# Optimization experiments

Measured on AMD Instinct MI355X. Metric: run time of the kernel, lower is better.

The kernel has to match this reference:

```python
import jax, jax.numpy as jnp
import numpy as np

B, L, H, F = 8, 1024, 512, 4

def setup_inputs() -> dict:
    key = jax.random.key(0)
    ks = jax.random.split(key, 5)
    x = jax.random.normal(ks[0], (B, L, H), dtype=jnp.float32)
    x_mask = jax.random.randint(ks[1], (B, L), 0, 2).astype(jnp.int32)
    W_proj = jax.random.normal(ks[2], (H, H * F), dtype=jnp.float32) * (1.0 / np.sqrt(H))
    b_proj = jnp.zeros((H * F,), dtype=jnp.float32)
    W_gate = jax.random.normal(ks[3], (2 * H, 2 * H), dtype=jnp.float32) * (1.0 / np.sqrt(2 * H))
    b_gate = jnp.zeros((2 * H,), dtype=jnp.float32)
    return {"x": x, "x_mask": x_mask, "W_proj": W_proj, "b_proj": b_proj,
            "W_gate": W_gate, "b_gate": b_gate}

def masked_softmax(logits, mask, eps=1e-13):
    # allennlp-style masked softmax used throughout sgnlp:
    # softmax(logits * mask) * mask, renormalized.
    m = mask.astype(logits.dtype)
    p = jax.nn.softmax(logits * m, axis=-1) * m
    return p / (p.sum(axis=-1, keepdims=True) + eps)

def reference(x, x_mask, W_proj, b_proj, W_gate, b_gate):
    b, l, h = x.shape
    # multi-factor projection: (B,L,H) -> (B,L,H,F) with relu (Linear activation='relu', dropout=0)
    y = jax.nn.relu(jnp.einsum('blh,hk->blk', x, W_proj) + b_proj)
    y = y.reshape(b, l, h, F)
    # per-factor self-attn scores stacked on last axis: (B,L,L,F)
    scores = jnp.einsum('blhf,bmhf->blmf', y, y)
    self_attn = scores.max(axis=-1)  # attn_pooling == 'max'
    # pairwise mask, zero diagonal
    mask = x_mask[:, :, None] * x_mask[:, None, :]
    mask = mask * (1 - jnp.eye(l, dtype=mask.dtype))
    alpha = masked_softmax(self_attn, mask)
    multi_attn_enc = jnp.einsum('blm,bmh->blh', alpha, x)
    joint = jnp.concatenate([x, multi_attn_enc], axis=-1)  # (B,L,2H)
    gate = jax.nn.sigmoid(jnp.einsum('blk,kj->blj', joint, W_gate) + b_gate)
    return gate * joint
```

## Files before the change

kernel.cpp:

```cpp
#include <hip/hip_runtime.h>


typedef _Float16 half8 __attribute__((ext_vector_type(8)));
typedef float floatx4 __attribute__((ext_vector_type(4)));

typedef const __attribute__((address_space(1))) void* gas_ptr;
typedef __attribute__((address_space(3))) void* las_ptr;

#define WAITV(n) asm volatile("s_waitcnt vmcnt(" #n ") lgkmcnt(0)" ::: "memory")


template<int NCH, int NT>
__device__ __forceinline__ void init_ptrs(const _Float16* src, int row0, int ld,
                                          const _Float16* gp[NCH]) {
  int t = threadIdx.x;
#pragma unroll
  for (int p = 0; p < NCH; ++p) {
    int c = p * NT + t;
    int row = c >> 3;
    int kg = c & 7;
    int gk = (kg ^ (row & 7)) << 3;
    gp[p] = src + (size_t)(row0 + row) * ld + gk;
  }
}


template<int NCH, int NT>
__device__ __forceinline__ void init_ptrs32(const _Float16* src, int row0, int ld,
                                            const _Float16* gp[NCH]) {
  int t = threadIdx.x;
#pragma unroll
  for (int p = 0; p < NCH; ++p) {
    int c = p * NT + t;
    int pair = c >> 3, s = c & 7;
    int q = s ^ (pair & 7);
    int row = row0 + pair * 2 + (q >> 2);
    int gk = (q & 3) << 3;
    gp[p] = src + (size_t)row * ld + gk;
  }
}

template<int NCH, int NT>
__device__ __forceinline__ void stage(const _Float16* const gp[NCH], _Float16* ldsbuf) {
  int t = threadIdx.x;
#pragma unroll
  for (int p = 0; p < NCH; ++p)
    __builtin_amdgcn_global_load_lds((gas_ptr)gp[p],
                                     (las_ptr)(ldsbuf + t * 8 + p * NT * 8), 16, 0, 0);
}

template<int NCH>
__device__ __forceinline__ void bump(const _Float16* gp[NCH], int d) {
#pragma unroll
  for (int p = 0; p < NCH; ++p) gp[p] += d;
}

__device__ __forceinline__ half8 frag_ld(const _Float16* lds, int row, int g) {
  return *(const half8*)(lds + row * 64 + ((g ^ (row & 7)) << 3));
}

__device__ __forceinline__ half8 frag_ld32(const _Float16* lds, int row, int kg) {
  int pair = row >> 1;
  int slot = (kg | ((row & 1) << 2)) ^ (pair & 7);
  return *(const half8*)(lds + pair * 64 + slot * 8);
}

__device__ __forceinline__ void kstep44(const _Float16* la, const _Float16* lb,
                                        floatx4 (&acc)[4][4], int ra, int rb, int quad) {
  half8 af[4], bf[4];
#pragma unroll
  for (int mi = 0; mi < 4; ++mi) af[mi] = frag_ld32(la, ra + mi * 16, quad);
#pragma unroll
  for (int ni = 0; ni < 4; ++ni) bf[ni] = frag_ld32(lb, rb + ni * 16, quad);
  __builtin_amdgcn_s_setprio(1);
#pragma unroll
  for (int mi = 0; mi < 4; ++mi)
#pragma unroll
    for (int ni = 0; ni < 4; ++ni)
      acc[mi][ni] = __builtin_amdgcn_mfma_f32_16x16x32_f16(af[mi], bf[ni], acc[mi][ni], 0, 0, 0);
  __builtin_amdgcn_s_setprio(0);
}

__device__ __forceinline__ void mfma_tile42(const _Float16* la, const _Float16* lb,
                                            floatx4 acc[4][2], int wm, int wn,
                                            int l16, int quad) {
#pragma unroll
  for (int kf = 0; kf < 2; ++kf) {
    half8 af[4], bf[2];
#pragma unroll
    for (int i = 0; i < 4; ++i) af[i] = frag_ld(la, wm * 64 + i * 16 + l16, kf * 4 + quad);
#pragma unroll
    for (int i = 0; i < 2; ++i) bf[i] = frag_ld(lb, wn * 32 + i * 16 + l16, kf * 4 + quad);
#pragma unroll
    for (int mi = 0; mi < 4; ++mi)
#pragma unroll
      for (int ni = 0; ni < 2; ++ni)
        acc[mi][ni] = __builtin_amdgcn_mfma_f32_16x16x32_f16(af[mi], bf[ni], acc[mi][ni], 0, 0, 0);
  }
}

#define ZERO_ACC44(acc)                                 \
  _Pragma("unroll") for (int mi = 0; mi < 4; ++mi)      \
  _Pragma("unroll") for (int ni = 0; ni < 4; ++ni)      \
  _Pragma("unroll") for (int r = 0; r < 4; ++r) acc[mi][ni][r] = 0.0f;

#define ZERO_ACC42(acc)                                 \
  _Pragma("unroll") for (int mi = 0; mi < 4; ++mi)      \
  _Pragma("unroll") for (int ni = 0; ni < 2; ++ni)      \
  _Pragma("unroll") for (int r = 0; r < 4; ++r) acc[mi][ni][r] = 0.0f;


__global__ __launch_bounds__(256) void prep_kernel(const float* __restrict__ xin,
                                                   _Float16* __restrict__ x16,
                                                   _Float16* __restrict__ xT,
                                                   const float* __restrict__ Wp,
                                                   _Float16* __restrict__ WpT,
                                                   const float* __restrict__ Wg,
                                                   _Float16* __restrict__ WgT) {
  __shared__ float tile[32][33];
  int id = blockIdx.x;
  int tx = threadIdx.x & 31, ty = threadIdx.x >> 5;
  if (id < 4096) {
    const int R = 1024, C = 512;
    int b = id & 7, rest = id >> 3;
    int c0 = (rest & 15) * 32, r0 = (rest >> 4) * 32;
    size_t boff = (size_t)b * R * C;
    const float* in = xin + boff;
    _Float16* o16 = x16 + boff;
    _Float16* oT = xT + boff;
#pragma unroll
    for (int i = 0; i < 32; i += 8) {
      float v = in[(size_t)(r0 + ty + i) * C + c0 + tx];
      tile[ty + i][tx] = v;
      o16[(size_t)(r0 + ty + i) * C + c0 + tx] = (_Float16)v;
    }
    __syncthreads();
#pragma unroll
    for (int i = 0; i < 32; i += 8)
      oT[(size_t)(c0 + ty + i) * R + r0 + tx] = (_Float16)tile[tx][ty + i];
  } else {
    int w = id - 4096;
    int bx = w & 63, by = (w >> 6) & 15, bz = w >> 10;
    const float* in; _Float16* out; int R, C, c0, r0;
    if (bz == 0) {
      in = Wp; out = WpT; R = 512; C = 2048;
      c0 = bx * 32; r0 = by * 32;
    } else {
      in = Wg; out = WgT; R = 1024; C = 1024;
      c0 = (bx & 31) * 32; r0 = (by * 2 + (bx >> 5)) * 32;
    }
#pragma unroll
    for (int i = 0; i < 32; i += 8)
      tile[ty + i][tx] = in[(size_t)(r0 + ty + i) * C + c0 + tx];
    __syncthreads();
#pragma unroll
    for (int i = 0; i < 32; i += 8) {
      int rr = c0 + ty + i;
      int prow = (bz == 0) ? ((rr & 3) * 512 + (rr >> 2)) : rr;
      out[(size_t)prow * R + r0 + tx] = (_Float16)tile[tx][ty + i];
    }
  }
}


__global__ __launch_bounds__(256, 2) void proj_kernel(const _Float16* __restrict__ x16,
                                                      const _Float16* __restrict__ WpT,
                                                      const float* __restrict__ bp,
                                                      _Float16* __restrict__ y_t) {
  __shared__ __align__(16) _Float16 ldsA[4][128 * 32];
  __shared__ __align__(16) _Float16 ldsB[4][128 * 32];
  int id = blockIdx.x;
  int xcd = id & 7, r = id >> 3;
  int i0 = (xcd * 8 + (r & 7)) * 128;
  int n0 = (r >> 3) * 128;
  int t = threadIdx.x, lane = t & 63, w = t >> 6;
  int wm = w >> 1, wn = w & 1, quad = lane >> 4, l16 = lane & 15;
  int ra = wm * 64 + l16, rb = wn * 64 + l16;
  const _Float16* gpA[2]; const _Float16* gpB[2];
  init_ptrs32<2, 256>(x16, i0, 512, gpA);
  init_ptrs32<2, 256>(WpT, n0, 512, gpB);
  floatx4 acc[4][4];
  ZERO_ACC44(acc);
  stage<2, 256>(gpA, ldsA[0]); bump<2>(gpA, 32);
  stage<2, 256>(gpB, ldsB[0]); bump<2>(gpB, 32);
  stage<2, 256>(gpA, ldsA[1]); bump<2>(gpA, 32);
  stage<2, 256>(gpB, ldsB[1]); bump<2>(gpB, 32);
  stage<2, 256>(gpA, ldsA[2]); bump<2>(gpA, 32);
  stage<2, 256>(gpB, ldsB[2]); bump<2>(gpB, 32);
#pragma unroll 1
  for (int u = 0; u < 13; ++u) {
    WAITV(8);
    __builtin_amdgcn_s_barrier();
    stage<2, 256>(gpA, ldsA[(u + 3) & 3]); bump<2>(gpA, 32);
    stage<2, 256>(gpB, ldsB[(u + 3) & 3]); bump<2>(gpB, 32);
    kstep44(ldsA[u & 3], ldsB[u & 3], acc, ra, rb, quad);
  }
  WAITV(8); __builtin_amdgcn_s_barrier(); kstep44(ldsA[1], ldsB[1], acc, ra, rb, quad);
  WAITV(4); __builtin_amdgcn_s_barrier(); kstep44(ldsA[2], ldsB[2], acc, ra, rb, quad);
  WAITV(0); __builtin_amdgcn_s_barrier(); kstep44(ldsA[3], ldsB[3], acc, ra, rb, quad);
#pragma unroll
  for (int mi = 0; mi < 4; ++mi)
#pragma unroll
    for (int ni = 0; ni < 4; ++ni)
#pragma unroll
      for (int r2 = 0; r2 < 4; ++r2) {
        int gr = i0 + wm * 64 + mi * 16 + quad * 4 + r2;
        int gc = n0 + wn * 64 + ni * 16 + l16;
        int f = gc >> 9, h = gc & 511;
        float c = fmaxf(acc[mi][ni][r2] + bp[h * 4 + f], 0.0f);
        int b = gr >> 10, l = gr & 1023;
        y_t[(((size_t)(b * 4 + f)) * 1024 + l) * 512 + h] = (_Float16)c;
      }
}


__global__ __launch_bounds__(256, 3) void score_kernel(const _Float16* __restrict__ y_t,
                                                       float* __restrict__ S) {
  __shared__ __align__(16) char smem[49152];
  _Float16* LA0 = (_Float16*)smem;
  _Float16* LA1 = (_Float16*)(smem + 16384);
  _Float16* LB0 = (_Float16*)(smem + 32768);
  _Float16* LB1 = (_Float16*)(smem + 40960);
  int id = blockIdx.x;
  int b = id & 7;
  int tt = id >> 3;
  int ti = 0;
  while (tt >= 16 - 2 * ti) { tt -= 16 - 2 * ti; ++ti; }
  int jh = 2 * ti + tt;
  int i0 = ti * 128, j0 = jh * 64;
  int t = threadIdx.x, lane = t & 63, w = t >> 6;
  int wm = w >> 1, wn = w & 1, quad = lane >> 4, l16 = lane & 15;
  const int PLANE = 1024 * 512;
  const _Float16* base = y_t + (size_t)b * 4 * PLANE;
  const _Float16* gpA[4]; const _Float16* gpB[2];
  init_ptrs<4, 256>(base, i0, 512, gpA);
  init_ptrs<2, 256>(base, j0, 512, gpB);
  floatx4 acc[4][2], smax[4][2];
  ZERO_ACC42(acc);
  stage<4, 256>(gpA, LA0); bump<4>(gpA, 64);
  stage<2, 256>(gpB, LB0); bump<2>(gpB, 64);
#pragma unroll 1
  for (int f = 0; f < 4; ++f) {
#pragma unroll 1
    for (int kt = 0; kt < 8; ++kt) {
      __syncthreads();
      if (f * 8 + kt < 31) {
        if (kt == 7) { bump<4>(gpA, PLANE - 512); bump<2>(gpB, PLANE - 512); }
        stage<4, 256>(gpA, ((kt + 1) & 1) ? LA1 : LA0); bump<4>(gpA, 64);
        stage<2, 256>(gpB, ((kt + 1) & 1) ? LB1 : LB0); bump<2>(gpB, 64);
      }
      mfma_tile42((kt & 1) ? LA1 : LA0, (kt & 1) ? LB1 : LB0, acc, wm, wn, l16, quad);
    }
    if (f == 0) {
#pragma unroll
      for (int mi = 0; mi < 4; ++mi)
#pragma unroll
        for (int ni = 0; ni < 2; ++ni) smax[mi][ni] = acc[mi][ni];
    } else {
#pragma unroll
      for (int mi = 0; mi < 4; ++mi)
#pragma unroll
        for (int ni = 0; ni < 2; ++ni)
#pragma unroll
          for (int r = 0; r < 4; ++r)
            smax[mi][ni][r] = fmaxf(smax[mi][ni][r], acc[mi][ni][r]);
    }
    ZERO_ACC42(acc);
  }
  float* Sb = S + (size_t)b * 1024 * 1024;
#pragma unroll
  for (int mi = 0; mi < 4; ++mi)
#pragma unroll
    for (int ni = 0; ni < 2; ++ni)
#pragma unroll
      for (int r = 0; r < 4; ++r) {
        int gi = i0 + wm * 64 + mi * 16 + quad * 4 + r;
        int gj = j0 + wn * 32 + ni * 16 + l16;
        Sb[(size_t)gi * 1024 + gj] = smax[mi][ni][r];
      }
  if (jh >= 2 * ti + 2) {
    __syncthreads();
    float* tl = (float*)smem;
#pragma unroll
    for (int mi = 0; mi < 4; ++mi)
#pragma unroll
      for (int ni = 0; ni < 2; ++ni)
#pragma unroll
        for (int r = 0; r < 4; ++r)
          tl[(wm * 64 + mi * 16 + quad * 4 + r) * 65 + (wn * 32 + ni * 16 + l16)] =
              smax[mi][ni][r];
    __syncthreads();
#pragma unroll 1
    for (int k = 0; k < 32; ++k) {
      int flat = k * 256 + t;
      int rm = flat >> 7, cm = flat & 127;
      Sb[(size_t)(j0 + rm) * 1024 + (i0 + cm)] = tl[cm * 65 + rm];
    }
  }
}


__global__ __launch_bounds__(256) void softmax_kernel(const float* __restrict__ S,
                                                      const int* __restrict__ xmask,
                                                      _Float16* __restrict__ alpha) {
  __shared__ float red[16];
  int id = blockIdx.x;
  int b = id & 7, l = id >> 3;
  int row = b * 1024 + l;
  const float* sr = S + (size_t)row * 1024;
  const int* mr = xmask + b * 1024;
  int t = threadIdx.x, lane = t & 63, wid = t >> 6;
  int rm = mr[l];
  float v[4], mm[4];
  float vmax = 0.0f;
#pragma unroll
  for (int q = 0; q < 4; ++q) {
    int i = t + q * 256;
    int m = (rm && mr[i] && (i != l)) ? 1 : 0;
    mm[q] = (float)m;
    v[q] = m ? sr[i] : 0.0f;
    vmax = fmaxf(vmax, v[q]);
  }
  for (int off = 32; off; off >>= 1) vmax = fmaxf(vmax, __shfl_down(vmax, off));
  if (lane == 0) red[wid] = vmax;
  __syncthreads();
  if (t == 0) red[8] = fmaxf(fmaxf(red[0], red[1]), fmaxf(red[2], red[3]));
  __syncthreads();
  vmax = red[8];
  float e[4], E = 0.0f, E2 = 0.0f;
#pragma unroll
  for (int q = 0; q < 4; ++q) {
    e[q] = expf(v[q] - vmax);
    E += e[q];
    E2 += e[q] * mm[q];
  }
  for (int off = 32; off; off >>= 1) {
    E += __shfl_down(E, off);
    E2 += __shfl_down(E2, off);
  }
  if (lane == 0) { red[wid] = E; red[4 + wid] = E2; }
  __syncthreads();
  if (t == 0) {
    red[9] = red[0] + red[1] + red[2] + red[3];
    red[10] = red[4] + red[5] + red[6] + red[7];
  }
  __syncthreads();
  E = red[9]; E2 = red[10];
  float inv = 1.0f / (E2 + 1e-13f * E);
  _Float16* ar = alpha + (size_t)row * 1024;
#pragma unroll
  for (int q = 0; q < 4; ++q) {
    int i = t + q * 256;
    ar[i] = (_Float16)(e[q] * mm[q] * inv);
  }
}


__global__ __launch_bounds__(256) void attn_kernel(const _Float16* __restrict__ alpha,
                                                   const _Float16* __restrict__ xT,
                                                   _Float16* __restrict__ enc) {
  __shared__ __align__(16) _Float16 ldsA[2][64 * 64];
  __shared__ __align__(16) _Float16 ldsB[2][128 * 64];
  int id = blockIdx.x;
  int b = id & 7;
  int r2 = id >> 3;
  int i0 = (r2 >> 2) * 64;
  int n0 = (r2 & 3) * 128;
  const _Float16* A = alpha + (size_t)b * 1024 * 1024;
  const _Float16* Bm = xT + (size_t)b * 512 * 1024;
  int t = threadIdx.x, lane = t & 63, wn = t >> 6;
  int quad = lane >> 4, l16 = lane & 15;
  const _Float16* gpA[2]; const _Float16* gpB[4];
  init_ptrs<2, 256>(A, i0, 1024, gpA);
  init_ptrs<4, 256>(Bm, n0, 1024, gpB);
  floatx4 acc[4][2];
  ZERO_ACC42(acc);
  stage<2, 256>(gpA, ldsA[0]); bump<2>(gpA, 64);
  stage<4, 256>(gpB, ldsB[0]); bump<4>(gpB, 64);
#pragma unroll 1
  for (int kt = 0; kt < 16; ++kt) {
    __syncthreads();
    if (kt < 15) {
      stage<2, 256>(gpA, ldsA[(kt + 1) & 1]); bump<2>(gpA, 64);
      stage<4, 256>(gpB, ldsB[(kt + 1) & 1]); bump<4>(gpB, 64);
    }
    const _Float16* la = ldsA[kt & 1];
    const _Float16* lb = ldsB[kt & 1];
#pragma unroll
    for (int kf = 0; kf < 2; ++kf) {
      half8 af[4], bf[2];
#pragma unroll
      for (int i = 0; i < 4; ++i) af[i] = frag_ld(la, i * 16 + l16, kf * 4 + quad);
#pragma unroll
      for (int i = 0; i < 2; ++i) bf[i] = frag_ld(lb, wn * 32 + i * 16 + l16, kf * 4 + quad);
#pragma unroll
      for (int mi = 0; mi < 4; ++mi)
#pragma unroll
        for (int ni = 0; ni < 2; ++ni)
          acc[mi][ni] = __builtin_amdgcn_mfma_f32_16x16x32_f16(af[mi], bf[ni], acc[mi][ni], 0, 0, 0);
    }
  }
  _Float16* eb = enc + (size_t)b * 1024 * 512;
#pragma unroll
  for (int mi = 0; mi < 4; ++mi)
#pragma unroll
    for (int ni = 0; ni < 2; ++ni)
#pragma unroll
      for (int r = 0; r < 4; ++r) {
        int gr = i0 + mi * 16 + quad * 4 + r;
        int gc = n0 + wn * 32 + ni * 16 + l16;
        eb[(size_t)gr * 512 + gc] = (_Float16)acc[mi][ni][r];
      }
}


__global__ __launch_bounds__(256, 2) void gate_kernel(const _Float16* __restrict__ x16,
                                                      const _Float16* __restrict__ enc,
                                                      const _Float16* __restrict__ WgT,
                                                      const float* __restrict__ bg,
                                                      float* __restrict__ out) {
  __shared__ __align__(16) _Float16 ldsA[4][128 * 32];
  __shared__ __align__(16) _Float16 ldsB[4][128 * 32];
  int id = blockIdx.x;
  int xcd = id & 7, r = id >> 3;
  int i0 = (xcd * 8 + (r & 7)) * 128;
  int n0 = (r >> 3) * 128;
  int t = threadIdx.x, lane = t & 63, w = t >> 6;
  int wm = w >> 1, wn = w & 1, quad = lane >> 4, l16 = lane & 15;
  int ra = wm * 64 + l16, rb = wn * 64 + l16;
  const _Float16* gpA[2]; const _Float16* gpA2[2]; const _Float16* gpB[2];
  init_ptrs32<2, 256>(x16, i0, 512, gpA);
  init_ptrs32<2, 256>(enc, i0, 512, gpA2);
  init_ptrs32<2, 256>(WgT, n0, 1024, gpB);
  floatx4 acc[4][4];
  ZERO_ACC44(acc);
  stage<2, 256>(gpA, ldsA[0]); bump<2>(gpA, 32);
  stage<2, 256>(gpB, ldsB[0]); bump<2>(gpB, 32);
  stage<2, 256>(gpA, ldsA[1]); bump<2>(gpA, 32);
  stage<2, 256>(gpB, ldsB[1]); bump<2>(gpB, 32);
  stage<2, 256>(gpA, ldsA[2]); bump<2>(gpA, 32);
  stage<2, 256>(gpB, ldsB[2]); bump<2>(gpB, 32);
#pragma unroll 1
  for (int u = 0; u < 29; ++u) {
    WAITV(8);
    __builtin_amdgcn_s_barrier();
    int v = u + 3;
    if (v < 16) { stage<2, 256>(gpA,  ldsA[v & 3]); bump<2>(gpA, 32); }
    else        { stage<2, 256>(gpA2, ldsA[v & 3]); bump<2>(gpA2, 32); }
    stage<2, 256>(gpB, ldsB[v & 3]); bump<2>(gpB, 32);
    kstep44(ldsA[u & 3], ldsB[u & 3], acc, ra, rb, quad);
  }
  WAITV(8); __builtin_amdgcn_s_barrier(); kstep44(ldsA[1], ldsB[1], acc, ra, rb, quad);
  WAITV(4); __builtin_amdgcn_s_barrier(); kstep44(ldsA[2], ldsB[2], acc, ra, rb, quad);
  WAITV(0); __builtin_amdgcn_s_barrier(); kstep44(ldsA[3], ldsB[3], acc, ra, rb, quad);
#pragma unroll
  for (int mi = 0; mi < 4; ++mi)
#pragma unroll
    for (int ni = 0; ni < 4; ++ni)
#pragma unroll
      for (int r2 = 0; r2 < 4; ++r2) {
        int gr = i0 + wm * 64 + mi * 16 + quad * 4 + r2;
        int gc = n0 + wn * 64 + ni * 16 + l16;
        float c = acc[mi][ni][r2] + bg[gc];
        float g = 1.0f / (1.0f + expf(-c));
        float jv = (gc < 512) ? (float)x16[(size_t)gr * 512 + gc]
                              : (float)enc[(size_t)gr * 512 + (gc - 512)];
        out[(size_t)gr * 1024 + gc] = g * jv;
      }
}


extern "C" void kernel_launch(void* const* d_in, const int* in_sizes, int n_in,
                              void* d_out, int out_size, void* d_ws, size_t ws_size,
                              hipStream_t stream) {
  const float* x  = (const float*)d_in[0];
  const int* xm   = (const int*)d_in[1];
  const float* Wp = (const float*)d_in[2];
  const float* bp = (const float*)d_in[3];
  const float* Wg = (const float*)d_in[4];
  const float* bg = (const float*)d_in[5];
  float* out = (float*)d_out;

  char* ws = (char*)d_ws;
  const size_t MB = 1024 * 1024;
  _Float16* x16 = (_Float16*)(ws);
  _Float16* xT  = (_Float16*)(ws + 8 * MB);
  _Float16* WpT = (_Float16*)(ws + 16 * MB);
  _Float16* WgT = (_Float16*)(ws + 18 * MB);
  _Float16* y_t = (_Float16*)(ws + 20 * MB);
  float*    S   = (float*)(ws + 52 * MB);
  _Float16* alpha = (_Float16*)(ws + 20 * MB);
  _Float16* enc   = (_Float16*)(ws + 36 * MB);

  prep_kernel<<<6144, 256, 0, stream>>>(x, x16, xT, Wp, WpT, Wg, WgT);

  proj_kernel<<<1024, 256, 0, stream>>>(x16, WpT, bp, y_t);
  score_kernel<<<576, 256, 0, stream>>>(y_t, S);
  softmax_kernel<<<8192, 256, 0, stream>>>(S, xm, alpha);
  attn_kernel<<<512, 256, 0, stream>>>(alpha, xT, enc);
  gate_kernel<<<512, 256, 0, stream>>>(x16, enc, WgT, bg, out);
}
```

Before: 213.5 us.

## Restructure proj and gate GEMMs into 512-thread larger-tile ping-pong pipelines

```diff
diff --git a/kernel.cpp b/kernel.cpp
--- a/kernel.cpp
+++ b/kernel.cpp
@@ -24,22 +24,6 @@
   }
 }
 
-
-template<int NCH, int NT>
-__device__ __forceinline__ void init_ptrs32(const _Float16* src, int row0, int ld,
-                                            const _Float16* gp[NCH]) {
-  int t = threadIdx.x;
-#pragma unroll
-  for (int p = 0; p < NCH; ++p) {
-    int c = p * NT + t;
-    int pair = c >> 3, s = c & 7;
-    int q = s ^ (pair & 7);
-    int row = row0 + pair * 2 + (q >> 2);
-    int gk = (q & 3) << 3;
-    gp[p] = src + (size_t)row * ld + gk;
-  }
-}
-
 template<int NCH, int NT>
 __device__ __forceinline__ void stage(const _Float16* const gp[NCH], _Float16* ldsbuf) {
   int t = threadIdx.x;
@@ -59,28 +43,6 @@
   return *(const half8*)(lds + row * 64 + ((g ^ (row & 7)) << 3));
 }
 
-__device__ __forceinline__ half8 frag_ld32(const _Float16* lds, int row, int kg) {
-  int pair = row >> 1;
-  int slot = (kg | ((row & 1) << 2)) ^ (pair & 7);
-  return *(const half8*)(lds + pair * 64 + slot * 8);
-}
-
-__device__ __forceinline__ void kstep44(const _Float16* la, const _Float16* lb,
-                                        floatx4 (&acc)[4][4], int ra, int rb, int quad) {
-  half8 af[4], bf[4];
-#pragma unroll
-  for (int mi = 0; mi < 4; ++mi) af[mi] = frag_ld32(la, ra + mi * 16, quad);
-#pragma unroll
-  for (int ni = 0; ni < 4; ++ni) bf[ni] = frag_ld32(lb, rb + ni * 16, quad);
-  __builtin_amdgcn_s_setprio(1);
-#pragma unroll
-  for (int mi = 0; mi < 4; ++mi)
-#pragma unroll
-    for (int ni = 0; ni < 4; ++ni)
-      acc[mi][ni] = __builtin_amdgcn_mfma_f32_16x16x32_f16(af[mi], bf[ni], acc[mi][ni], 0, 0, 0);
-  __builtin_amdgcn_s_setprio(0);
-}
-
 __device__ __forceinline__ void mfma_tile42(const _Float16* la, const _Float16* lb,
                                             floatx4 acc[4][2], int wm, int wn,
                                             int l16, int quad) {
@@ -98,16 +60,33 @@
         acc[mi][ni] = __builtin_amdgcn_mfma_f32_16x16x32_f16(af[mi], bf[ni], acc[mi][ni], 0, 0, 0);
   }
 }
-
-#define ZERO_ACC44(acc)                                 \
-  _Pragma("unroll") for (int mi = 0; mi < 4; ++mi)      \
-  _Pragma("unroll") for (int ni = 0; ni < 4; ++ni)      \
-  _Pragma("unroll") for (int r = 0; r < 4; ++r) acc[mi][ni][r] = 0.0f;
 
 #define ZERO_ACC42(acc)                                 \
   _Pragma("unroll") for (int mi = 0; mi < 4; ++mi)      \
   _Pragma("unroll") for (int ni = 0; ni < 2; ++ni)      \
   _Pragma("unroll") for (int r = 0; r < 4; ++r) acc[mi][ni][r] = 0.0f;
+
+#define MFMA_Q4(AF, BF, MB, NB)                                                  \
+  __builtin_amdgcn_s_setprio(1);                                                 \
+  _Pragma("unroll") for (int kf = 0; kf < 2; ++kf)                               \
+  _Pragma("unroll") for (int j = 0; j < 4; ++j)                                  \
+  _Pragma("unroll") for (int jn = 0; jn < 2; ++jn)                               \
+    acc[MB + j][NB + jn] = __builtin_amdgcn_mfma_f32_16x16x32_f16(               \
+        AF[kf * 4 + j], BF[kf * 2 + jn], acc[MB + j][NB + jn], 0, 0, 0);         \
+  __builtin_amdgcn_s_setprio(0);
+
+#define MFMA_Q2(AF, BF, MB, NB)                                                  \
+  __builtin_amdgcn_s_setprio(1);                                                 \
+  _Pragma("unroll") for (int kf = 0; kf < 2; ++kf)                               \
+  _Pragma("unroll") for (int j = 0; j < 2; ++j)                                  \
+  _Pragma("unroll") for (int jn = 0; jn < 2; ++jn)                               \
+    acc[MB + j][NB + jn] = __builtin_amdgcn_mfma_f32_16x16x32_f16(               \
+        AF[kf * 2 + j], BF[kf * 2 + jn], acc[MB + j][NB + jn], 0, 0, 0);         \
+  __builtin_amdgcn_s_setprio(0);
+
+#define PHASE_END()                      \
+  __builtin_amdgcn_s_barrier();          \
+  __builtin_amdgcn_sched_barrier(0)
 
 
 __global__ __launch_bounds__(256) void prep_kernel(const float* __restrict__ xin,
@@ -163,51 +142,101 @@
 }
 
 
-__global__ __launch_bounds__(256, 2) void proj_kernel(const _Float16* __restrict__ x16,
-                                                      const _Float16* __restrict__ WpT,
-                                                      const float* __restrict__ bp,
-                                                      _Float16* __restrict__ y_t) {
-  __shared__ __align__(16) _Float16 ldsA[4][128 * 32];
-  __shared__ __align__(16) _Float16 ldsB[4][128 * 32];
+__global__ __launch_bounds__(512) void proj_kernel(const _Float16* __restrict__ x16,
+                                                   const _Float16* __restrict__ WpT,
+                                                   const float* __restrict__ bp,
+                                                   _Float16* __restrict__ y_t) {
+  __shared__ __align__(16) _Float16 lA[2][2][128 * 64];
+  __shared__ __align__(16) _Float16 lB[2][2][128 * 64];
+  const int NK = 8;
   int id = blockIdx.x;
-  int xcd = id & 7, r = id >> 3;
-  int i0 = (xcd * 8 + (r & 7)) * 128;
-  int n0 = (r >> 3) * 128;
+  int xcd = id & 7, q = id >> 3;
+  int i0 = (xcd * 4 + (q & 3)) * 256;
+  int n0 = (q >> 2) * 256;
   int t = threadIdx.x, lane = t & 63, w = t >> 6;
-  int wm = w >> 1, wn = w & 1, quad = lane >> 4, l16 = lane & 15;
-  int ra = wm * 64 + l16, rb = wn * 64 + l16;
-  const _Float16* gpA[2]; const _Float16* gpB[2];
-  init_ptrs32<2, 256>(x16, i0, 512, gpA);
-  init_ptrs32<2, 256>(WpT, n0, 512, gpB);
-  floatx4 acc[4][4];
-  ZERO_ACC44(acc);
-  stage<2, 256>(gpA, ldsA[0]); bump<2>(gpA, 32);
-  stage<2, 256>(gpB, ldsB[0]); bump<2>(gpB, 32);
-  stage<2, 256>(gpA, ldsA[1]); bump<2>(gpA, 32);
-  stage<2, 256>(gpB, ldsB[1]); bump<2>(gpB, 32);
-  stage<2, 256>(gpA, ldsA[2]); bump<2>(gpA, 32);
-  stage<2, 256>(gpB, ldsB[2]); bump<2>(gpB, 32);
+  int wm = w >> 2, wn = w & 3;
+  int quad = lane >> 4, l16 = lane & 15;
+  int row0 = t >> 3, kg0 = t & 7;
+  int gk0 = (kg0 ^ (row0 & 7)) << 3;
+  int c1 = 512 + t, row1 = c1 >> 3, kg1 = c1 & 7;
+  int gk1 = (kg1 ^ (row1 & 7)) << 3;
+  const _Float16* Ab = x16 + (size_t)i0 * 512;
+  const _Float16* Bb = WpT + (size_t)n0 * 512;
+
+  auto stage_s = [&](int s) {
+    if (s >= 4 * NK) return;
+    int hs = s & 3, kt = s >> 2, buf = kt & 1;
+    int o = hs & 1, hf = hs >> 1;
+    const _Float16* src = (o ? Bb : Ab) + (size_t)(hf * 128) * 512 + kt * 64;
+    _Float16* dst = (o ? &lB[buf][hf][0] : &lA[buf][hf][0]) + t * 8;
+    __builtin_amdgcn_global_load_lds((gas_ptr)(src + (size_t)row0 * 512 + gk0),
+                                     (las_ptr)dst, 16, 0, 0);
+    __builtin_amdgcn_global_load_lds((gas_ptr)(src + (size_t)row1 * 512 + gk1),
+                                     (las_ptr)(dst + 4096), 16, 0, 0);
+  };
+
+  floatx4 acc[8][4];
+#pragma unroll
+  for (int mi = 0; mi < 8; ++mi)
+#pragma unroll
+    for (int ni = 0; ni < 4; ++ni)
+#pragma unroll
+      for (int r = 0; r < 4; ++r) acc[mi][ni][r] = 0.0f;
+
+  stage_s(0); stage_s(1); stage_s(2); stage_s(3); stage_s(4);
+  WAITV(2);
+  PHASE_END();
+
+  half8 af0[8], af1[8], bf0[4], bf1[4];
+  int brow = (wn & 1) * 64;
 #pragma unroll 1
-  for (int u = 0; u < 13; ++u) {
-    WAITV(8);
-    __builtin_amdgcn_s_barrier();
-    stage<2, 256>(gpA, ldsA[(u + 3) & 3]); bump<2>(gpA, 32);
-    stage<2, 256>(gpB, ldsB[(u + 3) & 3]); bump<2>(gpB, 32);
-    kstep44(ldsA[u & 3], ldsB[u & 3], acc, ra, rb, quad);
-  }
-  WAITV(8); __builtin_amdgcn_s_barrier(); kstep44(ldsA[1], ldsB[1], acc, ra, rb, quad);
-  WAITV(4); __builtin_amdgcn_s_barrier(); kstep44(ldsA[2], ldsB[2], acc, ra, rb, quad);
-  WAITV(0); __builtin_amdgcn_s_barrier(); kstep44(ldsA[3], ldsB[3], acc, ra, rb, quad);
-#pragma unroll
-  for (int mi = 0; mi < 4; ++mi)
+  for (int kt = 0; kt < NK; ++kt) {
+    int buf = kt & 1;
+    const _Float16* Ah = &lA[buf][wm][0];
+    const _Float16* Bh = &lB[buf][wn >> 1][0];
+#pragma unroll
+    for (int kf = 0; kf < 2; ++kf) {
+#pragma unroll
+      for (int j = 0; j < 4; ++j) af0[kf * 4 + j] = frag_ld(Ah, j * 16 + l16, kf * 4 + quad);
+#pragma unroll
+      for (int j = 0; j < 2; ++j) bf0[kf * 2 + j] = frag_ld(Bh, brow + j * 16 + l16, kf * 4 + quad);
+    }
+    MFMA_Q4(af0, bf0, 0, 0);
+    stage_s(4 * kt + 5);
+    PHASE_END();
+#pragma unroll
+    for (int kf = 0; kf < 2; ++kf)
+#pragma unroll
+      for (int j = 0; j < 2; ++j) bf1[kf * 2 + j] = frag_ld(Bh, brow + 32 + j * 16 + l16, kf * 4 + quad);
+    MFMA_Q4(af0, bf1, 0, 2);
+    stage_s(4 * kt + 6);
+    PHASE_END();
+#pragma unroll
+    for (int kf = 0; kf < 2; ++kf)
+#pragma unroll
+      for (int j = 0; j < 4; ++j) af1[kf * 4 + j] = frag_ld(Ah, 64 + j * 16 + l16, kf * 4 + quad);
+    MFMA_Q4(af1, bf1, 4, 2);
+    stage_s(4 * kt + 7);
+    PHASE_END();
+    MFMA_Q4(af1, bf0, 4, 0);
+    if (kt < NK - 2) {
+      stage_s(4 * kt + 8);
+      WAITV(2);
+    } else {
+      WAITV(0);
+    }
+    PHASE_END();
+  }
+#pragma unroll
+  for (int mi = 0; mi < 8; ++mi)
 #pragma unroll
     for (int ni = 0; ni < 4; ++ni)
 #pragma unroll
-      for (int r2 = 0; r2 < 4; ++r2) {
-        int gr = i0 + wm * 64 + mi * 16 + quad * 4 + r2;
+      for (int r = 0; r < 4; ++r) {
+        int gr = i0 + wm * 128 + mi * 16 + quad * 4 + r;
         int gc = n0 + wn * 64 + ni * 16 + l16;
         int f = gc >> 9, h = gc & 511;
-        float c = fmaxf(acc[mi][ni][r2] + bp[h * 4 + f], 0.0f);
+        float c = fmaxf(acc[mi][ni][r] + bp[h * 4 + f], 0.0f);
         int b = gr >> 10, l = gr & 1023;
         y_t[(((size_t)(b * 4 + f)) * 1024 + l) * 512 + h] = (_Float16)c;
       }
@@ -414,54 +443,112 @@
 }
 
 
-__global__ __launch_bounds__(256, 2) void gate_kernel(const _Float16* __restrict__ x16,
-                                                      const _Float16* __restrict__ enc,
-                                                      const _Float16* __restrict__ WgT,
-                                                      const float* __restrict__ bg,
-                                                      float* __restrict__ out) {
-  __shared__ __align__(16) _Float16 ldsA[4][128 * 32];
-  __shared__ __align__(16) _Float16 ldsB[4][128 * 32];
+__global__ __launch_bounds__(512) void gate_kernel(const _Float16* __restrict__ x16,
+                                                   const _Float16* __restrict__ enc,
+                                                   const _Float16* __restrict__ WgT,
+                                                   const float* __restrict__ bg,
+                                                   float* __restrict__ out) {
+  __shared__ __align__(16) _Float16 lA[2][128 * 64];
+  __shared__ __align__(16) _Float16 lB[2][2][128 * 64];
+  const int NK = 16;
   int id = blockIdx.x;
-  int xcd = id & 7, r = id >> 3;
-  int i0 = (xcd * 8 + (r & 7)) * 128;
-  int n0 = (r >> 3) * 128;
+  int xcd = id & 7, q = id >> 3;
+  int i0 = (xcd * 8 + (q & 7)) * 128;
+  int n0 = (q >> 3) * 256;
   int t = threadIdx.x, lane = t & 63, w = t >> 6;
-  int wm = w >> 1, wn = w & 1, quad = lane >> 4, l16 = lane & 15;
-  int ra = wm * 64 + l16, rb = wn * 64 + l16;
-  const _Float16* gpA[2]; const _Float16* gpA2[2]; const _Float16* gpB[2];
-  init_ptrs32<2, 256>(x16, i0, 512, gpA);
-  init_ptrs32<2, 256>(enc, i0, 512, gpA2);
-  init_ptrs32<2, 256>(WgT, n0, 1024, gpB);
+  int wm = w >> 2, wn = w & 3;
+  int quad = lane >> 4, l16 = lane & 15;
+  int row0 = t >> 3, kg0 = t & 7;
+  int gk0 = (kg0 ^ (row0 & 7)) << 3;
+  int c1 = 512 + t, row1 = c1 >> 3, kg1 = c1 & 7;
+  int gk1 = (kg1 ^ (row1 & 7)) << 3;
+  const _Float16* Ax = x16 + (size_t)i0 * 512;
+  const _Float16* Ae = enc + (size_t)i0 * 512;
+  const _Float16* Bb = WgT + (size_t)n0 * 1024;
+
+  auto stageA = [&](int kt) {
+    if (kt >= NK) return;
+    const _Float16* src = (kt < 8 ? Ax + kt * 64 : Ae + (kt - 8) * 64);
+    _Float16* dst = &lA[kt & 1][0] + t * 8;
+    __builtin_amdgcn_global_load_lds((gas_ptr)(src + (size_t)row0 * 512 + gk0),
+                                     (las_ptr)dst, 16, 0, 0);
+    __builtin_amdgcn_global_load_lds((gas_ptr)(src + (size_t)row1 * 512 + gk1),
+                                     (las_ptr)(dst + 4096), 16, 0, 0);
+  };
+  auto stageB = [&](int kt, int hf) {
+    if (kt >= NK) return;
+    const _Float16* src = Bb + (size_t)(hf * 128) * 1024 + kt * 64;
+    _Float16* dst = &lB[kt & 1][hf][0] + t * 8;
+    __builtin_amdgcn_global_load_lds((gas_ptr)(src + (size_t)row0 * 1024 + gk0),
+                                     (las_ptr)dst, 16, 0, 0);
+    __builtin_amdgcn_global_load_lds((gas_ptr)(src + (size_t)row1 * 1024 + gk1),
+                                     (las_ptr)(dst + 4096), 16, 0, 0);
+  };
+
   floatx4 acc[4][4];
-  ZERO_ACC44(acc);
-  stage<2, 256>(gpA, ldsA[0]); bump<2>(gpA, 32);
-  stage<2, 256>(gpB, ldsB[0]); bump<2>(gpB, 32);
-  stage<2, 256>(gpA, ldsA[1]); bump<2>(gpA, 32);
-  stage<2, 256>(gpB, ldsB[1]); bump<2>(gpB, 32);
-  stage<2, 256>(gpA, ldsA[2]); bump<2>(gpA, 32);
-  stage<2, 256>(gpB, ldsB[2]); bump<2>(gpB, 32);
+#pragma unroll
+  for (int mi = 0; mi < 4; ++mi)
+#pragma unroll
+    for (int ni = 0; ni < 4; ++ni)
+#pragma unroll
+      for (int r = 0; r < 4; ++r) acc[mi][ni][r] = 0.0f;
+
+  stageA(0); stageB(0, 0); stageB(0, 1);
+  stageA(1); stageB(1, 0); stageB(1, 1);
+  WAITV(6);
+  PHASE_END();
+
+  half8 af0[4], af1[4], bf0[4], bf1[4];
+  int arow = wm * 64, brow = (wn & 1) * 64;
 #pragma unroll 1
-  for (int u = 0; u < 29; ++u) {
-    WAITV(8);
-    __builtin_amdgcn_s_barrier();
-    int v = u + 3;
-    if (v < 16) { stage<2, 256>(gpA,  ldsA[v & 3]); bump<2>(gpA, 32); }
-    else        { stage<2, 256>(gpA2, ldsA[v & 3]); bump<2>(gpA2, 32); }
-    stage<2, 256>(gpB, ldsB[v & 3]); bump<2>(gpB, 32);
-    kstep44(ldsA[u & 3], ldsB[u & 3], acc, ra, rb, quad);
-  }
-  WAITV(8); __builtin_amdgcn_s_barrier(); kstep44(ldsA[1], ldsB[1], acc, ra, rb, quad);
-  WAITV(4); __builtin_amdgcn_s_barrier(); kstep44(ldsA[2], ldsB[2], acc, ra, rb, quad);
-  WAITV(0); __builtin_amdgcn_s_barrier(); kstep44(ldsA[3], ldsB[3], acc, ra, rb, quad);
+  for (int kt = 0; kt < NK; ++kt) {
+    int buf = kt & 1;
+    const _Float16* Ah = &lA[buf][0];
+    const _Float16* Bh = &lB[buf][wn >> 1][0];
+#pragma unroll
+    for (int kf = 0; kf < 2; ++kf) {
+#pragma unroll
+      for (int j = 0; j < 2; ++j) {
+        af0[kf * 2 + j] = frag_ld(Ah, arow + j * 16 + l16, kf * 4 + quad);
+        bf0[kf * 2 + j] = frag_ld(Bh, brow + j * 16 + l16, kf * 4 + quad);
+      }
+    }
+    MFMA_Q2(af0, bf0, 0, 0);
+    PHASE_END();
+#pragma unroll
+    for (int kf = 0; kf < 2; ++kf)
+#pragma unroll
+      for (int j = 0; j < 2; ++j)
+        af1[kf * 2 + j] = frag_ld(Ah, arow + 32 + j * 16 + l16, kf * 4 + quad);
+    MFMA_Q2(af1, bf0, 2, 0);
+    PHASE_END();
+#pragma unroll
+    for (int kf = 0; kf < 2; ++kf)
+#pragma unroll
+      for (int j = 0; j < 2; ++j)
+        bf1[kf * 2 + j] = frag_ld(Bh, brow + 32 + j * 16 + l16, kf * 4 + quad);
+    MFMA_Q2(af1, bf1, 2, 2);
+    stageA(kt + 2);
+    PHASE_END();
+    MFMA_Q2(af0, bf1, 0, 2);
+    if (kt < NK - 2) {
+      stageB(kt + 2, 0);
+      stageB(kt + 2, 1);
+      WAITV(6);
+    } else {
+      WAITV(0);
+    }
+    PHASE_END();
+  }
 #pragma unroll
   for (int mi = 0; mi < 4; ++mi)
 #pragma unroll
     for (int ni = 0; ni < 4; ++ni)
 #pragma unroll
-      for (int r2 = 0; r2 < 4; ++r2) {
-        int gr = i0 + wm * 64 + mi * 16 + quad * 4 + r2;
+      for (int r = 0; r < 4; ++r) {
+        int gr = i0 + wm * 64 + mi * 16 + quad * 4 + r;
         int gc = n0 + wn * 64 + ni * 16 + l16;
-        float c = acc[mi][ni][r2] + bg[gc];
+        float c = acc[mi][ni][r] + bg[gc];
         float g = 1.0f / (1.0f + expf(-c));
         float jv = (gc < 512) ? (float)x16[(size_t)gr * 512 + gc]
                               : (float)enc[(size_t)gr * 512 + (gc - 512)];
@@ -494,9 +581,9 @@
 
   prep_kernel<<<6144, 256, 0, stream>>>(x, x16, xT, Wp, WpT, Wg, WgT);
 
-  proj_kernel<<<1024, 256, 0, stream>>>(x16, WpT, bp, y_t);
+  proj_kernel<<<256, 512, 0, stream>>>(x16, WpT, bp, y_t);
   score_kernel<<<576, 256, 0, stream>>>(y_t, S);
   softmax_kernel<<<8192, 256, 0, stream>>>(S, xm, alpha);
   attn_kernel<<<512, 256, 0, stream>>>(alpha, xT, enc);
-  gate_kernel<<<512, 256, 0, stream>>>(x16, enc, WgT, bg, out);
-}
+  gate_kernel<<<256, 512, 0, stream>>>(x16, enc, WgT, bg, out);
+}
```

Result: faster. 207.9 us (-2.6%).
